# Kernel optimization log

Measured on AMD Instinct MI355X. Metric: run time of the kernel, lower is better.

The kernel has to match this reference:

```python
import jax, jax.numpy as jnp
import numpy as np

N = 50000; E = 800000; T = 800000; G = 64
H = 128; IEMB = 128; BAS = 8; NS = 4; NR = 6; OEH = 128; OUT = 1; NB = 4; CUT = 5.0


def envelope(x):
    # exponent=5 -> p=6: 1/x + a*x^5 + b*x^6 + c*x^7 with a=-28, b=48, c=-21
    return 1.0 / x - 28.0 * x**5 + 48.0 * x**6 - 21.0 * x**7


def setup_inputs() -> dict:
    key = jax.random.key(0)
    ks = iter(jax.random.split(key, 80))
    def w(shape, s=0.1):
        return jax.random.normal(next(ks), shape, dtype=jnp.float32) * s
    inp = {}
    inp['z'] = jax.random.randint(next(ks), (N,), 0, 100, dtype=jnp.int32)
    inp['dist'] = jax.random.uniform(next(ks), (E,), jnp.float32, 0.05, 1.0)
    inp['dist_trip'] = jax.random.uniform(next(ks), (T,), jnp.float32, 0.05, 1.0)
    inp['angle'] = jax.random.uniform(next(ks), (T,), jnp.float32, -1.0, 1.0)
    inp['edge_index'] = jax.random.randint(next(ks), (2, E), 0, N, dtype=jnp.int32)
    inp['triplets'] = jax.random.randint(next(ks), (T, 3), 0, N, dtype=jnp.int32)
    inp['batch'] = jnp.sort(jax.random.randint(next(ks), (N,), 0, G, dtype=jnp.int32))
    inp['atom_table'] = w((100, H), 1.0)
    inp['rbf_freq'] = jnp.arange(1, NR + 1, dtype=jnp.float32) * jnp.float32(np.pi)
    inp['sbf_freq'] = jnp.arange(1, NR + 1, dtype=jnp.float32) * jnp.float32(np.pi)
    inp['emb_w1'] = w((NR, IEMB)); inp['emb_b1'] = w((IEMB,), 0.01)
    inp['emb_w2'] = w((IEMB, H)); inp['emb_b2'] = w((H,), 0.01)
    inp['iw_rbf1'] = w((NB, NR, BAS)); inp['iw_rbf2'] = w((NB, BAS, H))
    inp['iw_sbf1'] = w((NB, NS * NR, BAS)); inp['iw_sbf2'] = w((NB, BAS, IEMB))
    inp['iw_t1'] = w((NB, H, IEMB)); inp['iw_t2'] = w((NB, IEMB, H)); inp['ib_t2'] = w((NB, H), 0.01)
    inp['iw_up'] = w((NB, H, H)); inp['ib_up'] = w((NB, H), 0.01)
    inp['iw_down'] = w((NB, H, H)); inp['ib_down'] = w((NB, H), 0.01)
    inp['ow_rbf'] = w((NB + 1, NR, H))
    inp['ow0'] = w((NB + 1, H, OEH)); inp['ob0'] = w((NB + 1, OEH), 0.01)
    inp['ow1'] = w((NB + 1, OEH, OEH)); inp['ob1'] = w((NB + 1, OEH), 0.01)
    inp['ow2'] = w((NB + 1, OEH, OUT)); inp['ob2'] = w((NB + 1, OUT), 0.01)
    return inp


def _forward(atom_table, rbf_freq, sbf_freq, emb_w1, emb_b1, emb_w2, emb_b2,
             iw_rbf1, iw_rbf2, iw_sbf1, iw_sbf2, iw_t1, iw_t2, ib_t2,
             iw_up, ib_up, iw_down, ib_down, ow_rbf, ow0, ob0, ow1, ob1, ow2, ob2,
             dist, dist_trip, angle, z, edge_index, triplets, batch):
    row, col = edge_index[0], edge_index[1]
    j_idx = triplets[:, 1]
    # radial basis for edges: [E, NR]
    d = dist[:, None] / CUT
    rbf_e = envelope(d) * jnp.sin(rbf_freq * d)
    # spherical basis for triplets: [T, NS*NR]
    dt = dist_trip[:, None] / CUT
    rbf_t = envelope(dt) * jnp.sin(sbf_freq * dt)
    a = angle[:, None]
    sph = jnp.concatenate([jnp.ones_like(a), a, 0.5 * (3 * a**2 - 1), 0.5 * (5 * a**3 - 3 * a)], axis=-1)
    sbf_t = (rbf_t[:, None, :] * sph[:, :, None]).reshape(a.shape[0], -1)

    x = atom_table[z]  # [N, H]
    # EmbeddingBlock: edge msg from rbf only, scattered to col
    e = jax.nn.silu(rbf_e @ emb_w1 + emb_b1) @ emb_w2 + emb_b2
    x = x + jax.ops.segment_sum(e, col, num_segments=N)

    def out_block(k, x):
        rbf_emb = rbf_e @ ow_rbf[k]            # [E, H]
        h = jax.ops.segment_sum(x[row] * rbf_emb, col, num_segments=N)
        h = jax.nn.silu(h @ ow0[k] + ob0[k])
        h = jax.nn.silu(h @ ow1[k] + ob1[k])
        return h @ ow2[k] + ob2[k]             # [N, OUT]

    P = out_block(0, x)
    for b in range(NB):
        x_up = x @ iw_up[b] + ib_up[b]
        x_down = x @ iw_down[b] + ib_down[b]
        rbf_emb = jax.nn.silu(rbf_e @ iw_rbf1[b]) @ iw_rbf2[b]      # [E, H]
        x_edge = x_up[row] * rbf_emb                                  # [E, H]
        sbf_emb = jax.nn.silu(sbf_t @ iw_sbf1[b]) @ iw_sbf2[b]      # [T, H]
        t = jax.nn.silu(x_down @ iw_t1[b]) @ iw_t2[b] + ib_t2[b]     # [N, H]
        # original: for each triplet i, x_edge += t[j]*sbf_emb[i] (broadcast over all edges)
        extra = jnp.sum(t[j_idx] * sbf_emb, axis=0)                   # [H]
        x_edge = x_edge + extra
        x = x + jax.ops.segment_sum(x_edge, col, num_segments=N)
        P = P + out_block(b + 1, x)

    counts = jax.ops.segment_sum(jnp.ones((x.shape[0],), jnp.float32), batch, num_segments=G)
    pooled = jax.ops.segment_sum(P, batch, num_segments=G) / jnp.maximum(counts, 1.0)[:, None]
    return pooled  # [G, OUT]


def reference(z, dist, dist_trip, angle, edge_index, triplets, batch, atom_table, rbf_freq, sbf_freq,
              emb_w1, emb_b1, emb_w2, emb_b2, iw_rbf1, iw_rbf2, iw_sbf1, iw_sbf2, iw_t1, iw_t2, ib_t2,
              iw_up, ib_up, iw_down, ib_down, ow_rbf, ow0, ob0, ow1, ob1, ow2, ob2):
    return _forward(atom_table, rbf_freq, sbf_freq, emb_w1, emb_b1, emb_w2, emb_b2,
                    iw_rbf1, iw_rbf2, iw_sbf1, iw_sbf2, iw_t1, iw_t2, ib_t2,
                    iw_up, ib_up, iw_down, ib_down, ow_rbf, ow0, ob0, ow1, ob1, ow2, ob2,
                    dist, dist_trip, angle, z, edge_index, triplets, batch)
```

## Files before the change

### kernel.cpp

```cpp
#include <hip/hip_runtime.h>
#include <hip/hip_fp16.h>

#define N_ 50000
#define E_ 800000
#define T_ 800000
#define G_ 64
#define H_ 128

#define NBK 782
#define NSB (NBK * 8)
#define CAPS 512
#define CHUNK 4096
#define EB ((E_ + CHUNK - 1) / CHUNK)
#define TB ((T_ + CHUNK - 1) / CHUNK)
#define XSLOT 16

typedef __attribute__((ext_vector_type(8))) short bf16x8;
typedef __attribute__((ext_vector_type(4))) float f32x4;
typedef _Float16 f16x2 __attribute__((ext_vector_type(2)));

__device__ __forceinline__ float siluf(float v) {
    return __fdividef(v, 1.0f + __expf(-v));
}

__device__ __forceinline__ unsigned short f2bf(float f) {
    unsigned int u = __float_as_uint(f);
    u += 0x7fffu + ((u >> 16) & 1u);
    return (unsigned short)(u >> 16);
}
__device__ __forceinline__ unsigned int f2bf2(float a, float b) {
    return (unsigned int)f2bf(a) | ((unsigned int)f2bf(b) << 16);
}
__device__ __forceinline__ float bf2f(unsigned short h) {
    return __uint_as_float(((unsigned int)h) << 16);
}
__device__ __forceinline__ float2 bf2x2(unsigned int p) {
    return make_float2(__uint_as_float(p << 16), __uint_as_float(p & 0xffff0000u));
}
__device__ __forceinline__ float fdot2f(f16x2 a, f16x2 b, float c) {
    return __builtin_amdgcn_fdot2(a, b, c, false);
}

__global__ __launch_bounds__(256) void k_bucket(const int* __restrict__ ecol,
                                                const int* __restrict__ trip,
                                                int* bcntE, unsigned int* __restrict__ ebkt,
                                                int* bcntT, unsigned int* __restrict__ tbkt) {
    __shared__ int hist[NBK];
    __shared__ int bbase[NBK];
    int blk = blockIdx.x;
    bool isE = blk < EB;
    int ebase = (isE ? blk : blk - EB) * CHUNK;
    const int nElem = isE ? E_ : T_;
    int r = blk & 7;
    int* bcnt = isE ? bcntE : bcntT;
    unsigned int* bkt = isE ? ebkt : tbkt;
    int tid = threadIdx.x;

    for (int i = tid; i < NBK; i += 256) hist[i] = 0;
    __syncthreads();

    int cols[16];
    #pragma unroll
    for (int u = 0; u < 16; ++u) {
        int idx = ebase + u * 256 + tid;
        int c = -1;
        if (idx < nElem) c = isE ? ecol[idx] : trip[3 * idx + 1];
        cols[u] = c;
        if (c >= 0) atomicAdd(&hist[c >> 6], 1);
    }
    __syncthreads();

    for (int b = tid; b < NBK; b += 256) {
        int c = hist[b];
        bbase[b] = c ? atomicAdd(&bcnt[b * 8 + r], c) : 0;
        hist[b] = 0;
    }
    __syncthreads();

    #pragma unroll
    for (int u = 0; u < 16; ++u) {
        int c = cols[u];
        if (c >= 0) {
            int bk = c >> 6;
            int off = atomicAdd(&hist[bk], 1);
            int pos = bbase[bk] + off;
            if (pos < CAPS) {
                int idx = ebase + u * 256 + tid;
                bkt[(size_t)(bk * 8 + r) * CAPS + pos] =
                    ((unsigned int)idx << 6) | (unsigned int)(c & 63);
            }
        }
    }
}

__global__ __launch_bounds__(1024) void k_scanB(const int* __restrict__ bcntE, int* bktbaseE,
                                                const int* __restrict__ bcntT, int* bktbaseT) {
    const int* bcnt = (blockIdx.x == 0) ? bcntE : bcntT;
    int* bb = (blockIdx.x == 0) ? bktbaseE : bktbaseT;
    int tid = threadIdx.x, lane = tid & 63, w = tid >> 6;
    __shared__ int wsum[16];
    int v = 0;
    if (tid < NBK) {
        #pragma unroll
        for (int s = 0; s < 8; ++s) v += min(bcnt[tid * 8 + s], CAPS);
    }
    int incl = v;
    #pragma unroll
    for (int s = 1; s < 64; s <<= 1) {
        int t = __shfl_up(incl, (unsigned)s, 64);
        if (lane >= s) incl += t;
    }
    if (lane == 63) wsum[w] = incl;
    __syncthreads();
    int wexcl = 0;
    for (int j = 0; j < w; ++j) wexcl += wsum[j];
    if (tid < NBK) bb[tid] = wexcl + incl - v;
}

__global__ __launch_bounds__(256) void k_place(const int* __restrict__ bcntE, const unsigned int* __restrict__ ebkt,
                                               const int* __restrict__ erow, const float* __restrict__ dist,
                                               const int* __restrict__ bktbaseE, int* __restrict__ rowptrE,
                                               int* __restrict__ slist, float* __restrict__ distS,
                                               const int* __restrict__ bcntT, const unsigned int* __restrict__ tbkt,
                                               const float* __restrict__ dist_trip, const float* __restrict__ angle,
                                               const int* __restrict__ bktbaseT, int* __restrict__ rowptrT,
                                               float2* __restrict__ tpay) {
    int b = blockIdx.x;
    bool isE = b < NBK;
    if (!isE) b -= NBK;
    int tid = threadIdx.x;
    __shared__ int ccnt[64];
    __shared__ int cbase[64];
    __shared__ int nb[8];
    if (tid < 64) ccnt[tid] = 0;
    const int* bcnt = isE ? bcntE : bcntT;
    const unsigned int* bkt = isE ? ebkt : tbkt;
    if (tid < 8) nb[tid] = min(bcnt[b * 8 + tid], CAPS);
    __syncthreads();
    for (int s = 0; s < 8; ++s) {
        int n = nb[s];
        const unsigned int* src = bkt + (size_t)(b * 8 + s) * CAPS;
        for (int i = tid; i < n; i += 256) atomicAdd(&ccnt[src[i] & 63u], 1);
    }
    __syncthreads();
    if (tid < 64) {
        int v = ccnt[tid];
        int incl = v;
        #pragma unroll
        for (int s = 1; s < 64; s <<= 1) {
            int t = __shfl_up(incl, (unsigned)s, 64);
            if (tid >= s) incl += t;
        }
        int base = (isE ? bktbaseE : bktbaseT)[b];
        int excl = base + incl - v;
        cbase[tid] = excl;
        int col = b * 64 + tid;
        int* rp = isE ? rowptrE : rowptrT;
        if (col <= N_) rp[col] = excl;
        ccnt[tid] = 0;
    }
    __syncthreads();
    for (int s = 0; s < 8; ++s) {
        int n = nb[s];
        const unsigned int* src = bkt + (size_t)(b * 8 + s) * CAPS;
        for (int i = tid; i < n; i += 256) {
            unsigned int rec = src[i];
            int c = (int)(rec & 63u);
            int e = (int)(rec >> 6);
            int off = atomicAdd(&ccnt[c], 1);
            int pos = cbase[c] + off;
            if (isE) {
                slist[pos] = erow[e];
                distS[pos] = dist[e];
            } else {
                tpay[pos] = make_float2(dist_trip[e], angle[e]);
            }
        }
    }
}

__global__ __launch_bounds__(256) void k_wprep(const float* __restrict__ emb_w2, const float* __restrict__ iw_down,
                                               const float* __restrict__ iw_t1, const float* __restrict__ iw_t2,
                                               const float* __restrict__ iw_up, const float* __restrict__ ow0,
                                               const float* __restrict__ ow1, unsigned short* __restrict__ Wt) {
    int mat = blockIdx.x >> 3;
    int part = blockIdx.x & 7;
    const float* src;
    if (mat == 0) src = emb_w2;
    else if (mat < 5) src = iw_down + (size_t)(mat - 1) * 16384;
    else if (mat < 9) src = iw_t1 + (size_t)(mat - 5) * 16384;
    else if (mat < 13) src = iw_t2 + (size_t)(mat - 9) * 16384;
    else if (mat < 17) src = iw_up + (size_t)(mat - 13) * 16384;
    else if (mat < 22) src = ow0 + (size_t)(mat - 17) * 16384;
    else src = ow1 + (size_t)(mat - 22) * 16384;
    unsigned short* dst = Wt + (size_t)mat * 16384;
    int base = part * 2048;
    for (int i = base + threadIdx.x; i < base + 2048; i += 256) {
        int k = i >> 7, n = i & 127;
        dst[n * 128 + k] = f2bf(src[i]);
    }
}

__global__ __launch_bounds__(256) void k_geom(const float* __restrict__ distS,
                                              const float* __restrict__ freq, const float* __restrict__ iw_rbf1,
                                              float* __restrict__ rbfS, __half* __restrict__ s8all, int n) {
    __shared__ float W1s[4][48];
    int tid = threadIdx.x;
    if (tid < 192) W1s[tid / 48][tid % 48] = iw_rbf1[tid];
    __syncthreads();
    int p = blockIdx.x * 256 + tid;
    if (p >= n) return;
    float d = distS[p] * 0.2f;
    float d2 = d * d, d4 = d2 * d2, d5 = d4 * d;
    float env = __fdividef(1.0f, d) - 28.0f * d5 + 48.0f * d5 * d - 21.0f * d5 * d2;
    float rb[6];
    #pragma unroll
    for (int r = 0; r < 6; ++r) {
        rb[r] = env * __sinf(freq[r] * d);
        rbfS[(size_t)p * 6 + r] = rb[r];
    }
    #pragma unroll
    for (int b = 0; b < 4; ++b) {
        __half out[8];
        #pragma unroll
        for (int k = 0; k < 8; ++k) {
            float u = 0.f;
            #pragma unroll
            for (int r = 0; r < 6; ++r) u += rb[r] * W1s[b][r * 8 + k];
            out[k] = __float2half(siluf(u));
        }
        *(uint4*)&s8all[((size_t)b * n + p) * 8] = *(uint4*)out;
    }
}

__global__ __launch_bounds__(256) void k_basis(const float2* __restrict__ tpay,
                                               const float* __restrict__ sfreq, __half* __restrict__ basis, int n) {
    int t = blockIdx.x * 256 + threadIdx.x;
    if (t >= n) return;
    float2 da = tpay[t];
    float d = da.x * 0.2f;
    float a = da.y;
    float d2 = d * d, d4 = d2 * d2, d5 = d4 * d;
    float env = __fdividef(1.0f, d) - 28.0f * d5 + 48.0f * d5 * d - 21.0f * d5 * d2;
    float rb[6];
    #pragma unroll
    for (int r = 0; r < 6; ++r) rb[r] = env * __sinf(sfreq[r] * d);
    float sph[4];
    sph[0] = 1.0f; sph[1] = a; sph[2] = 1.5f * a * a - 0.5f; sph[3] = 2.5f * a * a * a - 1.5f * a;
    __half out[24];
    #pragma unroll
    for (int s = 0; s < 4; ++s)
        #pragma unroll
        for (int r = 0; r < 6; ++r) out[s * 6 + r] = __float2half(sph[s] * rb[r]);
    uint4* dst = (uint4*)(basis + (size_t)t * 24);
    dst[0] = ((uint4*)out)[0];
    dst[1] = ((uint4*)out)[1];
    dst[2] = ((uint4*)out)[2];
}

__global__ __launch_bounds__(256) void k_sv4(const int* __restrict__ rowptrT, const __half* __restrict__ basis,
                                             const float* __restrict__ iw_sbf1, float* __restrict__ SV4, int n) {
    int wave = threadIdx.x >> 6, lane = threadIdx.x & 63;
    int node = blockIdx.x * 8 + wave * 2 + (lane >> 5);
    int sub = lane & 31;
    int blk = sub >> 3, k = sub & 7;
    if (node >= n) return;
    const float* W1 = iw_sbf1 + blk * 192;
    f16x2 w[12];
    #pragma unroll
    for (int j = 0; j < 12; ++j) {
        f16x2 t;
        t.x = (_Float16)W1[(2 * j) * 8 + k];
        t.y = (_Float16)W1[(2 * j + 1) * 8 + k];
        w[j] = t;
    }
    float acc = 0.f;
    int p0 = rowptrT[node], p1 = rowptrT[node + 1];
    for (int p = p0; p < p1; ++p) {
        union { uint4 q[3]; f16x2 h[12]; } bs;
        const uint4* bp = (const uint4*)(basis + (size_t)p * 24);
        bs.q[0] = bp[0]; bs.q[1] = bp[1]; bs.q[2] = bp[2];
        float u = 0.f;
        #pragma unroll
        for (int j = 0; j < 12; ++j) u = fdot2f(bs.h[j], w[j], u);
        acc += siluf(u);
    }
    SV4[((size_t)blk * n + node) * 8 + k] = acc;
}

__global__ __launch_bounds__(256) void k_init_x(const float* __restrict__ atab, const int* __restrict__ z,
                                                unsigned short* __restrict__ xh, int n) {
    int t = blockIdx.x * 256 + threadIdx.x;
    if (t >= n * 16) return;
    int node = t >> 4, q = t & 15;
    const float4* a4 = (const float4*)atab;
    float4 v0 = a4[(size_t)z[node] * 32 + q * 2];
    float4 v1 = a4[(size_t)z[node] * 32 + q * 2 + 1];
    uint4 pk;
    pk.x = f2bf2(v0.x, v0.y);
    pk.y = f2bf2(v0.z, v0.w);
    pk.z = f2bf2(v1.x, v1.y);
    pk.w = f2bf2(v1.z, v1.w);
    ((uint4*)xh)[t] = pk;
}

__global__ __launch_bounds__(256) void k_embS(const int* __restrict__ rowptr, const float* __restrict__ rbfS,
                                              const float* __restrict__ w1, const float* __restrict__ b1,
                                              unsigned short* __restrict__ SSh, int n) {
    int node = blockIdx.x * 4 + (threadIdx.x >> 6);
    int lane = threadIdx.x & 63;
    if (node >= n) return;
    int c = lane * 2;
    float wc0[6], wc1[6];
    #pragma unroll
    for (int r = 0; r < 6; ++r) { wc0[r] = w1[r * 128 + c]; wc1[r] = w1[r * 128 + c + 1]; }
    float bb0 = b1[c], bb1 = b1[c + 1];
    float a0 = 0.f, a1 = 0.f;
    int p0 = rowptr[node], p1 = rowptr[node + 1];
    for (int p = p0; p < p1; ++p) {
        const float2* r2 = (const float2*)&rbfS[(size_t)p * 6];
        float2 ra = r2[0], rbx = r2[1], rc = r2[2];
        float u0 = bb0 + ra.x * wc0[0] + ra.y * wc0[1] + rbx.x * wc0[2] + rbx.y * wc0[3] + rc.x * wc0[4] + rc.y * wc0[5];
        float u1 = bb1 + ra.x * wc1[0] + ra.y * wc1[1] + rbx.x * wc1[2] + rbx.y * wc1[3] + rc.x * wc1[4] + rc.y * wc1[5];
        a0 += siluf(u0);
        a1 += siluf(u1);
    }
    *(unsigned int*)&SSh[(size_t)node * 128 + c] = f2bf2(a0, a1);
}

template <int BIAS_MODE, bool SILU, bool ACCBF, bool ABF, bool WF32, bool WBF>
__global__ __launch_bounds__(128) void k_gemm_mfma(const void* __restrict__ Ap,
                                                   const unsigned short* __restrict__ Wt,
                                                   const float* __restrict__ bias, const int* __restrict__ rp,
                                                   float* __restrict__ C, unsigned short* __restrict__ Ch, int M) {
    int tid = threadIdx.x;
    int wave = tid >> 6, lane = tid & 63;
    int m15 = lane & 15, quad = lane >> 4;
    int row0 = blockIdx.x * 32 + wave * 16;
    int arow = row0 + m15;
    if (arow > M - 1) arow = M - 1;

    f32x4 acc[8];
    #pragma unroll
    for (int nt = 0; nt < 8; ++nt) acc[nt] = (f32x4){0.f, 0.f, 0.f, 0.f};

    #pragma unroll
    for (int kt = 0; kt < 4; ++kt) {
        int ks = kt * 32 + quad * 8;
        bf16x8 av;
        if constexpr (ABF) {
            av = *(const bf16x8*)((const unsigned short*)Ap + (size_t)arow * 128 + ks);
        } else {
            const float* Arow = (const float*)Ap + (size_t)arow * 128;
            float4 a0 = *(const float4*)(Arow + ks);
            float4 a1 = *(const float4*)(Arow + ks + 4);
            union { bf16x8 v; unsigned int u[4]; } af;
            af.u[0] = f2bf2(a0.x, a0.y);
            af.u[1] = f2bf2(a0.z, a0.w);
            af.u[2] = f2bf2(a1.x, a1.y);
            af.u[3] = f2bf2(a1.z, a1.w);
            av = af.v;
        }
        #pragma unroll
        for (int nt = 0; nt < 8; ++nt) {
            bf16x8 bf = *(const bf16x8*)(Wt + (size_t)(nt * 16 + m15) * 128 + ks);
            acc[nt] = __builtin_amdgcn_mfma_f32_16x16x32_bf16(av, bf, acc[nt], 0, 0, 0);
        }
    }

    #pragma unroll
    for (int nt = 0; nt < 8; ++nt) {
        int col = nt * 16 + m15;
        float bc = 0.f;
        if constexpr (BIAS_MODE != 0) bc = bias[col];
        #pragma unroll
        for (int reg = 0; reg < 4; ++reg) {
            int row = row0 + quad * 4 + reg;
            if (row < M) {
                float v = acc[nt][reg];
                if constexpr (BIAS_MODE == 1) v += bc;
                if constexpr (BIAS_MODE == 2) v += bc * (float)(rp[row + 1] - rp[row]);
                if constexpr (SILU) v = siluf(v);
                if constexpr (ACCBF) v += bf2f(Ch[(size_t)row * 128 + col]);
                if constexpr (WF32) C[(size_t)row * 128 + col] = v;
                if constexpr (WBF) Ch[(size_t)row * 128 + col] = f2bf(v);
            }
        }
    }
}

template <int PACC>
__global__ __launch_bounds__(128) void k_out_mlp(const unsigned short* __restrict__ hB,
                                                 const unsigned short* __restrict__ W0t, const float* __restrict__ b0,
                                                 const unsigned short* __restrict__ W1t, const float* __restrict__ b1,
                                                 const float* __restrict__ w2col, const float* __restrict__ ob2p,
                                                 float* __restrict__ Pout, int M) {
    __shared__ unsigned short lds[2][16 * 136];
    int tid = threadIdx.x;
    int wave = tid >> 6, lane = tid & 63;
    int m15 = lane & 15, quad = lane >> 4;
    int row0 = blockIdx.x * 32 + wave * 16;
    int arow = row0 + m15;
    if (arow > M - 1) arow = M - 1;
    unsigned short* L = lds[wave];

    f32x4 acc[8];
    #pragma unroll
    for (int nt = 0; nt < 8; ++nt) acc[nt] = (f32x4){0.f, 0.f, 0.f, 0.f};
    #pragma unroll
    for (int kt = 0; kt < 4; ++kt) {
        int ks = kt * 32 + quad * 8;
        bf16x8 av = *(const bf16x8*)(hB + (size_t)arow * 128 + ks);
        #pragma unroll
        for (int nt = 0; nt < 8; ++nt) {
            bf16x8 bf = *(const bf16x8*)(W0t + (size_t)(nt * 16 + m15) * 128 + ks);
            acc[nt] = __builtin_amdgcn_mfma_f32_16x16x32_bf16(av, bf, acc[nt], 0, 0, 0);
        }
    }
    #pragma unroll
    for (int nt = 0; nt < 8; ++nt) {
        int col = nt * 16 + m15;
        float bc = b0[col];
        #pragma unroll
        for (int reg = 0; reg < 4; ++reg)
            L[(quad * 4 + reg) * 136 + col] = f2bf(siluf(acc[nt][reg] + bc));
    }
    __syncthreads();

    #pragma unroll
    for (int nt = 0; nt < 8; ++nt) acc[nt] = (f32x4){0.f, 0.f, 0.f, 0.f};
    #pragma unroll
    for (int kt = 0; kt < 4; ++kt) {
        int ks = kt * 32 + quad * 8;
        bf16x8 av = *(const bf16x8*)(L + m15 * 136 + ks);
        #pragma unroll
        for (int nt = 0; nt < 8; ++nt) {
            bf16x8 bf = *(const bf16x8*)(W1t + (size_t)(nt * 16 + m15) * 128 + ks);
            acc[nt] = __builtin_amdgcn_mfma_f32_16x16x32_bf16(av, bf, acc[nt], 0, 0, 0);
        }
    }
    float w2c[8], pp[4];
    #pragma unroll
    for (int nt = 0; nt < 8; ++nt) w2c[nt] = w2col[nt * 16 + m15];
    #pragma unroll
    for (int reg = 0; reg < 4; ++reg) pp[reg] = 0.f;
    #pragma unroll
    for (int nt = 0; nt < 8; ++nt) {
        float bc = b1[nt * 16 + m15];
        #pragma unroll
        for (int reg = 0; reg < 4; ++reg)
            pp[reg] += siluf(acc[nt][reg] + bc) * w2c[nt];
    }
    #pragma unroll
    for (int reg = 0; reg < 4; ++reg) {
        float s = pp[reg];
        s += __shfl_xor(s, 1, 64);
        s += __shfl_xor(s, 2, 64);
        s += __shfl_xor(s, 4, 64);
        s += __shfl_xor(s, 8, 64);
        if (m15 == 0) {
            int row = row0 + quad * 4 + reg;
            if (row < M) {
                float r = s + ob2p[0];
                if constexpr (PACC == 2) r += Pout[row];
                Pout[row] = r;
            }
        }
    }
}

__global__ __launch_bounds__(128) void k_block_mlp(const unsigned short* __restrict__ xh,
                                                   const unsigned short* __restrict__ Wd, const float* __restrict__ bd,
                                                   const unsigned short* __restrict__ Wt1,
                                                   const unsigned short* __restrict__ Wt2, const float* __restrict__ bt2,
                                                   const unsigned short* __restrict__ Wup, const float* __restrict__ bup,
                                                   const float* __restrict__ SV, const float* __restrict__ W2,
                                                   float* __restrict__ extraP,
                                                   unsigned short* __restrict__ xuph, int M) {
    __shared__ union {
        unsigned short h[2][16 * 136];
        float f[32 * 132];
    } sm;
    int tid = threadIdx.x;
    int wave = tid >> 6, lane = tid & 63;
    int m15 = lane & 15, quad = lane >> 4;
    int row0 = blockIdx.x * 32 + wave * 16;
    int arow = row0 + m15;
    if (arow > M - 1) arow = M - 1;
    unsigned short* L = sm.h[wave];

    f32x4 accD[8], accU[8];
    #pragma unroll
    for (int nt = 0; nt < 8; ++nt) { accD[nt] = (f32x4){0.f, 0.f, 0.f, 0.f}; accU[nt] = (f32x4){0.f, 0.f, 0.f, 0.f}; }
    #pragma unroll
    for (int kt = 0; kt < 4; ++kt) {
        int ks = kt * 32 + quad * 8;
        bf16x8 av = *(const bf16x8*)(xh + (size_t)arow * 128 + ks);
        #pragma unroll
        for (int nt = 0; nt < 8; ++nt) {
            bf16x8 bd_ = *(const bf16x8*)(Wd + (size_t)(nt * 16 + m15) * 128 + ks);
            accD[nt] = __builtin_amdgcn_mfma_f32_16x16x32_bf16(av, bd_, accD[nt], 0, 0, 0);
            bf16x8 bu_ = *(const bf16x8*)(Wup + (size_t)(nt * 16 + m15) * 128 + ks);
            accU[nt] = __builtin_amdgcn_mfma_f32_16x16x32_bf16(av, bu_, accU[nt], 0, 0, 0);
        }
    }
    #pragma unroll
    for (int nt = 0; nt < 8; ++nt) {
        int col = nt * 16 + m15;
        float bcu = bup[col], bcd = bd[col];
        #pragma unroll
        for (int reg = 0; reg < 4; ++reg) {
            int row = row0 + quad * 4 + reg;
            if (row < M) xuph[(size_t)row * 128 + col] = f2bf(accU[nt][reg] + bcu);
            L[(quad * 4 + reg) * 136 + col] = f2bf(accD[nt][reg] + bcd);
        }
    }
    __syncthreads();

    #pragma unroll
    for (int nt = 0; nt < 8; ++nt) accD[nt] = (f32x4){0.f, 0.f, 0.f, 0.f};
    #pragma unroll
    for (int kt = 0; kt < 4; ++kt) {
        int ks = kt * 32 + quad * 8;
        bf16x8 av = *(const bf16x8*)(L + m15 * 136 + ks);
        #pragma unroll
        for (int nt = 0; nt < 8; ++nt) {
            bf16x8 bf = *(const bf16x8*)(Wt1 + (size_t)(nt * 16 + m15) * 128 + ks);
            accD[nt] = __builtin_amdgcn_mfma_f32_16x16x32_bf16(av, bf, accD[nt], 0, 0, 0);
        }
    }
    __syncthreads();
    #pragma unroll
    for (int nt = 0; nt < 8; ++nt) {
        int col = nt * 16 + m15;
        #pragma unroll
        for (int reg = 0; reg < 4; ++reg)
            L[(quad * 4 + reg) * 136 + col] = f2bf(siluf(accD[nt][reg]));
    }
    __syncthreads();

    #pragma unroll
    for (int nt = 0; nt < 8; ++nt) accD[nt] = (f32x4){0.f, 0.f, 0.f, 0.f};
    #pragma unroll
    for (int kt = 0; kt < 4; ++kt) {
        int ks = kt * 32 + quad * 8;
        bf16x8 av = *(const bf16x8*)(L + m15 * 136 + ks);
        #pragma unroll
        for (int nt = 0; nt < 8; ++nt) {
            bf16x8 bf = *(const bf16x8*)(Wt2 + (size_t)(nt * 16 + m15) * 128 + ks);
            accD[nt] = __builtin_amdgcn_mfma_f32_16x16x32_bf16(av, bf, accD[nt], 0, 0, 0);
        }
    }
    __syncthreads();
    #pragma unroll
    for (int nt = 0; nt < 8; ++nt) {
        int col = nt * 16 + m15;
        float bc = bt2[col];
        #pragma unroll
        for (int reg = 0; reg < 4; ++reg) {
            int lr = wave * 16 + quad * 4 + reg;
            sm.f[lr * 132 + col] = accD[nt][reg] + bc;
        }
    }
    __syncthreads();

    int col = tid;
    float acc8[8];
    #pragma unroll
    for (int k = 0; k < 8; ++k) acc8[k] = 0.f;
    int rmax = M - blockIdx.x * 32;
    if (rmax > 32) rmax = 32;
    for (int rr = 0; rr < rmax; ++rr) {
        float t = sm.f[rr * 132 + col];
        const float4* sv4 = (const float4*)&SV[(size_t)(blockIdx.x * 32 + rr) * 8];
        float4 s0 = sv4[0], s1 = sv4[1];
        acc8[0] += t * s0.x; acc8[1] += t * s0.y; acc8[2] += t * s0.z; acc8[3] += t * s0.w;
        acc8[4] += t * s1.x; acc8[5] += t * s1.y; acc8[6] += t * s1.z; acc8[7] += t * s1.w;
    }
    float e = 0.f;
    #pragma unroll
    for (int k = 0; k < 8; ++k) e += acc8[k] * W2[k * 128 + col];
    atomicAdd(&extraP[(blockIdx.x & (XSLOT - 1)) * 128 + col], e);
}

__global__ __launch_bounds__(256) void k_out_gather(const int* __restrict__ rowptr, const int* __restrict__ slist,
                                                    const float* __restrict__ rbfS,
                                                    const unsigned short* __restrict__ xh,
                                                    const float* __restrict__ wrbf,
                                                    unsigned short* __restrict__ hB, int n) {
    int node = blockIdx.x * 4 + (threadIdx.x >> 6);
    int lane = threadIdx.x & 63;
    if (node >= n) return;
    int c = lane * 2;
    float wc0[6], wc1[6];
    #pragma unroll
    for (int r = 0; r < 6; ++r) { wc0[r] = wrbf[r * 128 + c]; wc1[r] = wrbf[r * 128 + c + 1]; }
    float a0 = 0.f, a1 = 0.f;
    int p0 = rowptr[node], p1 = rowptr[node + 1];
    int p = p0;
    for (; p + 4 <= p1; p += 4) {
        int s0 = slist[p], s1 = slist[p + 1], s2 = slist[p + 2], s3 = slist[p + 3];
        float2 rb[4][3];
        #pragma unroll
        for (int u = 0; u < 4; ++u) {
            const float2* r2 = (const float2*)&rbfS[(size_t)(p + u) * 6];
            rb[u][0] = r2[0]; rb[u][1] = r2[1]; rb[u][2] = r2[2];
        }
        unsigned int xv0 = *(const unsigned int*)&xh[(size_t)s0 * 128 + c];
        unsigned int xv1 = *(const unsigned int*)&xh[(size_t)s1 * 128 + c];
        unsigned int xv2 = *(const unsigned int*)&xh[(size_t)s2 * 128 + c];
        unsigned int xv3 = *(const unsigned int*)&xh[(size_t)s3 * 128 + c];
        #pragma unroll
        for (int u = 0; u < 4; ++u) {
            float e0 = rb[u][0].x * wc0[0] + rb[u][0].y * wc0[1] + rb[u][1].x * wc0[2] +
                       rb[u][1].y * wc0[3] + rb[u][2].x * wc0[4] + rb[u][2].y * wc0[5];
            float e1 = rb[u][0].x * wc1[0] + rb[u][0].y * wc1[1] + rb[u][1].x * wc1[2] +
                       rb[u][1].y * wc1[3] + rb[u][2].x * wc1[4] + rb[u][2].y * wc1[5];
            float2 xf = bf2x2((u == 0) ? xv0 : (u == 1) ? xv1 : (u == 2) ? xv2 : xv3);
            a0 += xf.x * e0;
            a1 += xf.y * e1;
        }
    }
    for (; p < p1; ++p) {
        int src = slist[p];
        const float2* r2 = (const float2*)&rbfS[(size_t)p * 6];
        float2 ra = r2[0], rbx = r2[1], rc = r2[2];
        float e0 = ra.x * wc0[0] + ra.y * wc0[1] + rbx.x * wc0[2] + rbx.y * wc0[3] + rc.x * wc0[4] + rc.y * wc0[5];
        float e1 = ra.x * wc1[0] + ra.y * wc1[1] + rbx.x * wc1[2] + rbx.y * wc1[3] + rc.x * wc1[4] + rc.y * wc1[5];
        float2 xf = bf2x2(*(const unsigned int*)&xh[(size_t)src * 128 + c]);
        a0 += xf.x * e0;
        a1 += xf.y * e1;
    }
    *(unsigned int*)&hB[(size_t)node * 128 + c] = f2bf2(a0, a1);
}

__global__ __launch_bounds__(256) void k_interact(const int* __restrict__ rowptr, const int* __restrict__ slist,
                                                  const __half* __restrict__ s8, const float* __restrict__ W2,
                                                  const float* __restrict__ extraP,
                                                  const unsigned short* __restrict__ xuph,
                                                  unsigned short* __restrict__ xh, int n) {
    __shared__ float exs[128];
    int tid = threadIdx.x;
    if (tid < 128) {
        float s = 0.f;
        #pragma unroll
        for (int q = 0; q < XSLOT; ++q) s += extraP[q * 128 + tid];
        exs[tid] = s;
    }
    __syncthreads();
    int node = blockIdx.x * 4 + (tid >> 6);
    int lane = tid & 63;
    if (node >= n) return;
    int c = lane * 2;
    f16x2 w2a[4], w2b[4];
    #pragma unroll
    for (int j = 0; j < 4; ++j) {
        f16x2 wa, wb;
        wa.x = (_Float16)W2[(2 * j) * 128 + c];
        wa.y = (_Float16)W2[(2 * j + 1) * 128 + c];
        wb.x = (_Float16)W2[(2 * j) * 128 + c + 1];
        wb.y = (_Float16)W2[(2 * j + 1) * 128 + c + 1];
        w2a[j] = wa;
        w2b[j] = wb;
    }
    int p0 = rowptr[node], p1 = rowptr[node + 1];
    float cntf = (float)(p1 - p0);
    float a0 = cntf * exs[c], a1 = cntf * exs[c + 1];
    int p = p0;
    for (; p + 4 <= p1; p += 4) {
        int s0 = slist[p], s1 = slist[p + 1], s2 = slist[p + 2], s3 = slist[p + 3];
        uint4 sv[4];
        #pragma unroll
        for (int u = 0; u < 4; ++u) sv[u] = *(const uint4*)(s8 + (size_t)(p + u) * 8);
        unsigned int xv0 = *(const unsigned int*)&xuph[(size_t)s0 * 128 + c];
        unsigned int xv1 = *(const unsigned int*)&xuph[(size_t)s1 * 128 + c];
        unsigned int xv2 = *(const unsigned int*)&xuph[(size_t)s2 * 128 + c];
        unsigned int xv3 = *(const unsigned int*)&xuph[(size_t)s3 * 128 + c];
        #pragma unroll
        for (int u = 0; u < 4; ++u) {
            union { uint4 q; f16x2 h[4]; } s;
            s.q = sv[u];
            float e0 = fdot2f(s.h[0], w2a[0], 0.f);
            e0 = fdot2f(s.h[1], w2a[1], e0);
            e0 = fdot2f(s.h[2], w2a[2], e0);
            e0 = fdot2f(s.h[3], w2a[3], e0);
            float e1 = fdot2f(s.h[0], w2b[0], 0.f);
            e1 = fdot2f(s.h[1], w2b[1], e1);
            e1 = fdot2f(s.h[2], w2b[2], e1);
            e1 = fdot2f(s.h[3], w2b[3], e1);
            float2 xf = bf2x2((u == 0) ? xv0 : (u == 1) ? xv1 : (u == 2) ? xv2 : xv3);
            a0 += xf.x * e0;
            a1 += xf.y * e1;
        }
    }
    for (; p < p1; ++p) {
        int src = slist[p];
        float2 xf = bf2x2(*(const unsigned int*)&xuph[(size_t)src * 128 + c]);
        union { uint4 q; f16x2 h[4]; } s;
        s.q = *(const uint4*)(s8 + (size_t)p * 8);
        float e0 = fdot2f(s.h[0], w2a[0], 0.f);
        e0 = fdot2f(s.h[1], w2a[1], e0);
        e0 = fdot2f(s.h[2], w2a[2], e0);
        e0 = fdot2f(s.h[3], w2a[3], e0);
        float e1 = fdot2f(s.h[0], w2b[0], 0.f);
        e1 = fdot2f(s.h[1], w2b[1], e1);
        e1 = fdot2f(s.h[2], w2b[2], e1);
        e1 = fdot2f(s.h[3], w2b[3], e1);
        a0 += xf.x * e0;
        a1 += xf.y * e1;
    }
    unsigned int cur = *(unsigned int*)&xh[(size_t)node * 128 + c];
    float2 xc = bf2x2(cur);
    *(unsigned int*)&xh[(size_t)node * 128 + c] = f2bf2(xc.x + a0, xc.y + a1);
}

__global__ __launch_bounds__(256) void k_pool(const float* __restrict__ P, const int* __restrict__ batch,
                                              float* __restrict__ pool, float* __restrict__ cnt, int n) {
    int i = blockIdx.x * 256 + threadIdx.x;
    int lane = threadIdx.x & 63;
    int b = (i < n) ? batch[i] : -1;
    float p = (i < n) ? P[i] : 0.f;
    int b0 = __shfl(b, 0, 64);
    int b63 = __shfl(b, 63, 64);
    if (b0 == b63 && b0 >= 0) {
        float s = p;
        #pragma unroll
        for (int off = 32; off > 0; off >>= 1) s += __shfl_xor(s, off, 64);
        if (lane == 0) {
            atomicAdd(&pool[b0], s);
            atomicAdd(&cnt[b0], 64.0f);
        }
    } else {
        if (i < n) {
            atomicAdd(&pool[b], p);
            atomicAdd(&cnt[b], 1.0f);
        }
    }
}

__global__ __launch_bounds__(64) void k_final(const float* __restrict__ pool, const float* __restrict__ cnt,
                                              float* __restrict__ out) {
    int g = threadIdx.x;
    if (g < G_) out[g] = __fdividef(pool[g], fmaxf(cnt[g], 1.0f));
}

extern "C" void kernel_launch(void* const* d_in, const int* in_sizes, int n_in,
                              void* d_out, int out_size, void* d_ws, size_t ws_size,
                              hipStream_t stream) {
    (void)in_sizes; (void)n_in; (void)out_size; (void)ws_size;
    const int* z = (const int*)d_in[0];
    const float* dist = (const float*)d_in[1];
    const float* dist_trip = (const float*)d_in[2];
    const float* angle = (const float*)d_in[3];
    const int* edge_index = (const int*)d_in[4];
    const int* triplets = (const int*)d_in[5];
    const int* batch = (const int*)d_in[6];
    const float* atom_table = (const float*)d_in[7];
    const float* rbf_freq = (const float*)d_in[8];
    const float* sbf_freq = (const float*)d_in[9];
    const float* emb_w1 = (const float*)d_in[10];
    const float* emb_b1 = (const float*)d_in[11];
    const float* emb_w2 = (const float*)d_in[12];
    const float* emb_b2 = (const float*)d_in[13];
    const float* iw_rbf1 = (const float*)d_in[14];
    const float* iw_rbf2 = (const float*)d_in[15];
    const float* iw_sbf1 = (const float*)d_in[16];
    const float* iw_sbf2 = (const float*)d_in[17];
    const float* iw_t1 = (const float*)d_in[18];
    const float* iw_t2 = (const float*)d_in[19];
    const float* ib_t2 = (const float*)d_in[20];
    const float* iw_up = (const float*)d_in[21];
    const float* ib_up = (const float*)d_in[22];
    const float* iw_down = (const float*)d_in[23];
    const float* ib_down = (const float*)d_in[24];
    const float* ow_rbf = (const float*)d_in[25];
    const float* ow0 = (const float*)d_in[26];
    const float* ob0 = (const float*)d_in[27];
    const float* ow1 = (const float*)d_in[28];
    const float* ob1 = (const float*)d_in[29];
    const float* ow2 = (const float*)d_in[30];
    const float* ob2 = (const float*)d_in[31];

    const int* erow = edge_index;
    const int* ecol = edge_index + E_;

    float* ws = (float*)d_ws;
    float* bufA = ws;
    float* bufB = bufA + (size_t)N_ * H_;
    float* P = bufB + (size_t)N_ * H_;
    float* rbfS = P + N_;
    float* SV4 = rbfS + (size_t)E_ * 6;
    float* extra4 = SV4 + (size_t)4 * N_ * 8;
    float* pool = extra4 + 4 * XSLOT * 128;
    float* cnt = pool + G_;
    int* bcntE = (int*)(cnt + G_);
    int* bcntT = bcntE + NSB;
    int* bktbaseE = bcntT + NSB;
    int* bktbaseT = bktbaseE + NBK;
    int* rowptr = bktbaseT + NBK;
    int* rowptrT = rowptr + N_ + 1;
    int* slist = rowptrT + N_ + 1;
    float* distS = (float*)(slist + E_);
    uintptr_t tp = (uintptr_t)(distS + E_);
    tp = (tp + 7) & ~(uintptr_t)7;
    float2* tpay = (float2*)tp;
    __half* s8all = (__half*)(tpay + T_);
    __half* basis = s8all + (size_t)4 * E_ * 8;
    unsigned short* xh = (unsigned short*)(basis + (size_t)T_ * 24);
    unsigned short* xuph = xh + (size_t)N_ * H_;
    unsigned short* Wt = xuph + (size_t)N_ * H_;
    unsigned short* hB = (unsigned short*)bufB;

    unsigned int* ebkt = (unsigned int*)s8all;
    unsigned int* tbkt = ebkt + (size_t)NSB * CAPS;

    const int EG = (E_ + 255) / 256;
    const int TG = (T_ + 255) / 256;
    const int NG4 = (N_ + 3) / 4;
    const int GEMMG2 = (N_ + 31) / 32;

    hipMemsetAsync(extra4, 0, (4 * XSLOT * 128 + 2 * G_ + 2 * NSB) * sizeof(float), stream);
    k_wprep<<<27 * 8, 256, 0, stream>>>(emb_w2, iw_down, iw_t1, iw_t2, iw_up, ow0, ow1, Wt);
    k_bucket<<<EB + TB, 256, 0, stream>>>(ecol, triplets, bcntE, ebkt, bcntT, tbkt);
    k_scanB<<<2, 1024, 0, stream>>>(bcntE, bktbaseE, bcntT, bktbaseT);
    k_place<<<2 * NBK, 256, 0, stream>>>(bcntE, ebkt, erow, dist, bktbaseE, rowptr, slist, distS,
                                         bcntT, tbkt, dist_trip, angle, bktbaseT, rowptrT, tpay);

    k_geom<<<EG, 256, 0, stream>>>(distS, rbf_freq, iw_rbf1, rbfS, s8all, E_);
    k_basis<<<TG, 256, 0, stream>>>(tpay, sbf_freq, basis, T_);
    k_sv4<<<(N_ + 7) / 8, 256, 0, stream>>>(rowptrT, basis, iw_sbf1, SV4, N_);
    k_init_x<<<(N_ * 16 + 255) / 256, 256, 0, stream>>>(atom_table, z, xh, N_);

    k_embS<<<NG4, 256, 0, stream>>>(rowptr, rbfS, emb_w1, emb_b1, (unsigned short*)bufA, N_);
    k_gemm_mfma<2, false, true, true, false, true><<<GEMMG2, 128, 0, stream>>>(
        bufA, Wt, emb_b2, rowptr, nullptr, xh, N_);

    auto out_block = [&](int k, bool first) {
        k_out_gather<<<NG4, 256, 0, stream>>>(rowptr, slist, rbfS, xh,
                                              ow_rbf + (size_t)k * 6 * 128, hB, N_);
        if (first)
            k_out_mlp<1><<<GEMMG2, 128, 0, stream>>>(hB, Wt + (size_t)(17 + k) * 16384, ob0 + k * 128,
                                                     Wt + (size_t)(22 + k) * 16384, ob1 + k * 128,
                                                     ow2 + k * 128, ob2 + k, P, N_);
        else
            k_out_mlp<2><<<GEMMG2, 128, 0, stream>>>(hB, Wt + (size_t)(17 + k) * 16384, ob0 + k * 128,
                                                     Wt + (size_t)(22 + k) * 16384, ob1 + k * 128,
                                                     ow2 + k * 128, ob2 + k, P, N_);
    };

    out_block(0, true);

    for (int b = 0; b < 4; ++b) {
        k_block_mlp<<<GEMMG2, 128, 0, stream>>>(xh,
                                                Wt + (size_t)(1 + b) * 16384, ib_down + b * 128,
                                                Wt + (size_t)(5 + b) * 16384,
                                                Wt + (size_t)(9 + b) * 16384, ib_t2 + b * 128,
                                                Wt + (size_t)(13 + b) * 16384, ib_up + b * 128,
                                                SV4 + (size_t)b * N_ * 8,
                                                iw_sbf2 + (size_t)b * 1024,
                                                extra4 + (size_t)b * XSLOT * 128,
                                                xuph, N_);
        k_interact<<<NG4, 256, 0, stream>>>(rowptr, slist, s8all + (size_t)b * E_ * 8,
                                            iw_rbf2 + (size_t)b * 1024, extra4 + (size_t)b * XSLOT * 128,
                                            xuph, xh, N_);
        out_block(b + 1, false);
    }

    k_pool<<<(N_ + 255) / 256, 256, 0, stream>>>(P, batch, pool, cnt, N_);
    k_final<<<1, 64, 0, stream>>>(pool, cnt, (float*)d_out);
}
```

Before: 1.441 ms.

## Merge independent kernels into combined launches to overlap work across the pipeline

```diff
diff --git a/kernel.cpp b/kernel.cpp
--- a/kernel.cpp
+++ b/kernel.cpp
@@ -14,6 +14,13 @@
 #define EB ((E_ + CHUNK - 1) / CHUNK)
 #define TB ((T_ + CHUNK - 1) / CHUNK)
 #define XSLOT 16
+
+#define GEMMG2 ((N_ + 31) / 32)
+#define NG2 ((N_ + 1) / 2)
+#define NIX ((N_ * 16 + 127) / 128)
+#define SVG ((N_ + 3) / 4)
+#define EG ((E_ + 255) / 256)
+#define TG ((T_ + 255) / 256)
 
 typedef __attribute__((ext_vector_type(8))) short bf16x8;
 typedef __attribute__((ext_vector_type(4))) float f32x4;
@@ -201,67 +208,168 @@
     }
 }
 
-__global__ __launch_bounds__(256) void k_geom(const float* __restrict__ distS,
-                                              const float* __restrict__ freq, const float* __restrict__ iw_rbf1,
-                                              float* __restrict__ rbfS, __half* __restrict__ s8all, int n) {
+__global__ __launch_bounds__(256) void k_geomb(const float* __restrict__ distS,
+                                               const float* __restrict__ freq, const float* __restrict__ iw_rbf1,
+                                               float* __restrict__ rbfS, __half* __restrict__ s8all,
+                                               const float2* __restrict__ tpay, const float* __restrict__ sfreq,
+                                               __half* __restrict__ basis) {
     __shared__ float W1s[4][48];
     int tid = threadIdx.x;
-    if (tid < 192) W1s[tid / 48][tid % 48] = iw_rbf1[tid];
-    __syncthreads();
-    int p = blockIdx.x * 256 + tid;
-    if (p >= n) return;
-    float d = distS[p] * 0.2f;
-    float d2 = d * d, d4 = d2 * d2, d5 = d4 * d;
-    float env = __fdividef(1.0f, d) - 28.0f * d5 + 48.0f * d5 * d - 21.0f * d5 * d2;
-    float rb[6];
-    #pragma unroll
-    for (int r = 0; r < 6; ++r) {
-        rb[r] = env * __sinf(freq[r] * d);
-        rbfS[(size_t)p * 6 + r] = rb[r];
-    }
-    #pragma unroll
-    for (int b = 0; b < 4; ++b) {
-        __half out[8];
-        #pragma unroll
-        for (int k = 0; k < 8; ++k) {
-            float u = 0.f;
+    if (blockIdx.x < EG) {
+        if (tid < 192) W1s[tid / 48][tid % 48] = iw_rbf1[tid];
+        __syncthreads();
+        int p = blockIdx.x * 256 + tid;
+        if (p >= E_) return;
+        float d = distS[p] * 0.2f;
+        float d2 = d * d, d4 = d2 * d2, d5 = d4 * d;
+        float env = __fdividef(1.0f, d) - 28.0f * d5 + 48.0f * d5 * d - 21.0f * d5 * d2;
+        float rb[6];
+        #pragma unroll
+        for (int r = 0; r < 6; ++r) {
+            rb[r] = env * __sinf(freq[r] * d);
+            rbfS[(size_t)p * 6 + r] = rb[r];
+        }
+        #pragma unroll
+        for (int b = 0; b < 4; ++b) {
+            __half out[8];
             #pragma unroll
-            for (int r = 0; r < 6; ++r) u += rb[r] * W1s[b][r * 8 + k];
-            out[k] = __float2half(siluf(u));
-        }
-        *(uint4*)&s8all[((size_t)b * n + p) * 8] = *(uint4*)out;
-    }
-}
-
-__global__ __launch_bounds__(256) void k_basis(const float2* __restrict__ tpay,
-                                               const float* __restrict__ sfreq, __half* __restrict__ basis, int n) {
-    int t = blockIdx.x * 256 + threadIdx.x;
-    if (t >= n) return;
-    float2 da = tpay[t];
-    float d = da.x * 0.2f;
-    float a = da.y;
-    float d2 = d * d, d4 = d2 * d2, d5 = d4 * d;
-    float env = __fdividef(1.0f, d) - 28.0f * d5 + 48.0f * d5 * d - 21.0f * d5 * d2;
-    float rb[6];
-    #pragma unroll
-    for (int r = 0; r < 6; ++r) rb[r] = env * __sinf(sfreq[r] * d);
-    float sph[4];
-    sph[0] = 1.0f; sph[1] = a; sph[2] = 1.5f * a * a - 0.5f; sph[3] = 2.5f * a * a * a - 1.5f * a;
-    __half out[24];
-    #pragma unroll
-    for (int s = 0; s < 4; ++s)
-        #pragma unroll
-        for (int r = 0; r < 6; ++r) out[s * 6 + r] = __float2half(sph[s] * rb[r]);
-    uint4* dst = (uint4*)(basis + (size_t)t * 24);
-    dst[0] = ((uint4*)out)[0];
-    dst[1] = ((uint4*)out)[1];
-    dst[2] = ((uint4*)out)[2];
-}
-
-__global__ __launch_bounds__(256) void k_sv4(const int* __restrict__ rowptrT, const __half* __restrict__ basis,
-                                             const float* __restrict__ iw_sbf1, float* __restrict__ SV4, int n) {
-    int wave = threadIdx.x >> 6, lane = threadIdx.x & 63;
-    int node = blockIdx.x * 8 + wave * 2 + (lane >> 5);
+            for (int k = 0; k < 8; ++k) {
+                float u = 0.f;
+                #pragma unroll
+                for (int r = 0; r < 6; ++r) u += rb[r] * W1s[b][r * 8 + k];
+                out[k] = __float2half(siluf(u));
+            }
+            *(uint4*)&s8all[((size_t)b * E_ + p) * 8] = *(uint4*)out;
+        }
+    } else {
+        int t = (blockIdx.x - EG) * 256 + tid;
+        if (t >= T_) return;
+        float2 da = tpay[t];
+        float d = da.x * 0.2f;
+        float a = da.y;
+        float d2 = d * d, d4 = d2 * d2, d5 = d4 * d;
+        float env = __fdividef(1.0f, d) - 28.0f * d5 + 48.0f * d5 * d - 21.0f * d5 * d2;
+        float rb[6];
+        #pragma unroll
+        for (int r = 0; r < 6; ++r) rb[r] = env * __sinf(sfreq[r] * d);
+        float sph[4];
+        sph[0] = 1.0f; sph[1] = a; sph[2] = 1.5f * a * a - 0.5f; sph[3] = 2.5f * a * a * a - 1.5f * a;
+        __half out[24];
+        #pragma unroll
+        for (int s = 0; s < 4; ++s)
+            #pragma unroll
+            for (int r = 0; r < 6; ++r) out[s * 6 + r] = __float2half(sph[s] * rb[r]);
+        uint4* dst = (uint4*)(basis + (size_t)t * 24);
+        dst[0] = ((uint4*)out)[0];
+        dst[1] = ((uint4*)out)[1];
+        dst[2] = ((uint4*)out)[2];
+    }
+}
+
+__global__ __launch_bounds__(128) void k_embSix(const float* __restrict__ atab, const int* __restrict__ z,
+                                                unsigned short* __restrict__ xh,
+                                                const int* __restrict__ rowptr, const float* __restrict__ rbfS,
+                                                const float* __restrict__ w1, const float* __restrict__ b1,
+                                                unsigned short* __restrict__ SSh) {
+    int tid = threadIdx.x;
+    if (blockIdx.x < NIX) {
+        int t = blockIdx.x * 128 + tid;
+        if (t >= N_ * 16) return;
+        int node = t >> 4, q = t & 15;
+        const float4* a4 = (const float4*)atab;
+        float4 v0 = a4[(size_t)z[node] * 32 + q * 2];
+        float4 v1 = a4[(size_t)z[node] * 32 + q * 2 + 1];
+        uint4 pk;
+        pk.x = f2bf2(v0.x, v0.y);
+        pk.y = f2bf2(v0.z, v0.w);
+        pk.z = f2bf2(v1.x, v1.y);
+        pk.w = f2bf2(v1.z, v1.w);
+        ((uint4*)xh)[t] = pk;
+    } else {
+        int node = (blockIdx.x - NIX) * 2 + (tid >> 6);
+        int lane = tid & 63;
+        if (node >= N_) return;
+        int c = lane * 2;
+        float wc0[6], wc1[6];
+        #pragma unroll
+        for (int r = 0; r < 6; ++r) { wc0[r] = w1[r * 128 + c]; wc1[r] = w1[r * 128 + c + 1]; }
+        float bb0 = b1[c], bb1 = b1[c + 1];
+        float a0 = 0.f, a1 = 0.f;
+        int p0 = rowptr[node], p1 = rowptr[node + 1];
+        int p = p0;
+        for (; p + 4 <= p1; p += 4) {
+            float2 rb[4][3];
+            #pragma unroll
+            for (int u = 0; u < 4; ++u) {
+                const float2* r2 = (const float2*)&rbfS[(size_t)(p + u) * 6];
+                rb[u][0] = r2[0]; rb[u][1] = r2[1]; rb[u][2] = r2[2];
+            }
+            #pragma unroll
+            for (int u = 0; u < 4; ++u) {
+                float u0 = bb0 + rb[u][0].x * wc0[0] + rb[u][0].y * wc0[1] + rb[u][1].x * wc0[2] +
+                           rb[u][1].y * wc0[3] + rb[u][2].x * wc0[4] + rb[u][2].y * wc0[5];
+                float u1 = bb1 + rb[u][0].x * wc1[0] + rb[u][0].y * wc1[1] + rb[u][1].x * wc1[2] +
+                           rb[u][1].y * wc1[3] + rb[u][2].x * wc1[4] + rb[u][2].y * wc1[5];
+                a0 += siluf(u0);
+                a1 += siluf(u1);
+            }
+        }
+        for (; p < p1; ++p) {
+            const float2* r2 = (const float2*)&rbfS[(size_t)p * 6];
+            float2 ra = r2[0], rbx = r2[1], rc = r2[2];
+            float u0 = bb0 + ra.x * wc0[0] + ra.y * wc0[1] + rbx.x * wc0[2] + rbx.y * wc0[3] + rc.x * wc0[4] + rc.y * wc0[5];
+            float u1 = bb1 + ra.x * wc1[0] + ra.y * wc1[1] + rbx.x * wc1[2] + rbx.y * wc1[3] + rc.x * wc1[4] + rc.y * wc1[5];
+            a0 += siluf(u0);
+            a1 += siluf(u1);
+        }
+        *(unsigned int*)&SSh[(size_t)node * 128 + c] = f2bf2(a0, a1);
+    }
+}
+
+
+__device__ __forceinline__ void body_gemm(int bid, const unsigned short* Ap, const unsigned short* Wt,
+                                          const float* bias, const int* rp, unsigned short* Ch, int M) {
+    int tid = threadIdx.x;
+    int wave = tid >> 6, lane = tid & 63;
+    int m15 = lane & 15, quad = lane >> 4;
+    int row0 = bid * 32 + wave * 16;
+    int arow = row0 + m15;
+    if (arow > M - 1) arow = M - 1;
+
+    f32x4 acc[8];
+    #pragma unroll
+    for (int nt = 0; nt < 8; ++nt) acc[nt] = (f32x4){0.f, 0.f, 0.f, 0.f};
+    #pragma unroll
+    for (int kt = 0; kt < 4; ++kt) {
+        int ks = kt * 32 + quad * 8;
+        bf16x8 av = *(const bf16x8*)(Ap + (size_t)arow * 128 + ks);
+        #pragma unroll
+        for (int nt = 0; nt < 8; ++nt) {
+            bf16x8 bf = *(const bf16x8*)(Wt + (size_t)(nt * 16 + m15) * 128 + ks);
+            acc[nt] = __builtin_amdgcn_mfma_f32_16x16x32_bf16(av, bf, acc[nt], 0, 0, 0);
+        }
+    }
+    #pragma unroll
+    for (int nt = 0; nt < 8; ++nt) {
+        int col = nt * 16 + m15;
+        float bc = bias[col];
+        #pragma unroll
+        for (int reg = 0; reg < 4; ++reg) {
+            int row = row0 + quad * 4 + reg;
+            if (row < M) {
+                float v = acc[nt][reg] + bc * (float)(rp[row + 1] - rp[row]);
+                v += bf2f(Ch[(size_t)row * 128 + col]);
+                Ch[(size_t)row * 128 + col] = f2bf(v);
+            }
+        }
+    }
+}
+
+__device__ __forceinline__ void body_sv4(int bid, const int* rowptrT, const __half* basis,
+                                         const float* iw_sbf1, float* SV4, int n) {
+    int tid = threadIdx.x;
+    int wave = tid >> 6, lane = tid & 63;
+    int node = bid * 4 + wave * 2 + (lane >> 5);
     int sub = lane & 31;
     int blk = sub >> 3, k = sub & 7;
     if (node >= n) return;
@@ -288,121 +396,178 @@
     SV4[((size_t)blk * n + node) * 8 + k] = acc;
 }
 
-__global__ __launch_bounds__(256) void k_init_x(const float* __restrict__ atab, const int* __restrict__ z,
-                                                unsigned short* __restrict__ xh, int n) {
-    int t = blockIdx.x * 256 + threadIdx.x;
-    if (t >= n * 16) return;
-    int node = t >> 4, q = t & 15;
-    const float4* a4 = (const float4*)atab;
-    float4 v0 = a4[(size_t)z[node] * 32 + q * 2];
-    float4 v1 = a4[(size_t)z[node] * 32 + q * 2 + 1];
-    uint4 pk;
-    pk.x = f2bf2(v0.x, v0.y);
-    pk.y = f2bf2(v0.z, v0.w);
-    pk.z = f2bf2(v1.x, v1.y);
-    pk.w = f2bf2(v1.z, v1.w);
-    ((uint4*)xh)[t] = pk;
-}
-
-__global__ __launch_bounds__(256) void k_embS(const int* __restrict__ rowptr, const float* __restrict__ rbfS,
-                                              const float* __restrict__ w1, const float* __restrict__ b1,
-                                              unsigned short* __restrict__ SSh, int n) {
-    int node = blockIdx.x * 4 + (threadIdx.x >> 6);
-    int lane = threadIdx.x & 63;
+__device__ __forceinline__ void body_gather(int node0, const int* rowptr, const int* slist,
+                                            const float* rbfS, const unsigned short* xh,
+                                            const float* wrbf, unsigned short* hB, int n) {
+    int tid = threadIdx.x;
+    int node = node0 + (tid >> 6);
+    int lane = tid & 63;
     if (node >= n) return;
     int c = lane * 2;
     float wc0[6], wc1[6];
     #pragma unroll
-    for (int r = 0; r < 6; ++r) { wc0[r] = w1[r * 128 + c]; wc1[r] = w1[r * 128 + c + 1]; }
-    float bb0 = b1[c], bb1 = b1[c + 1];
+    for (int r = 0; r < 6; ++r) { wc0[r] = wrbf[r * 128 + c]; wc1[r] = wrbf[r * 128 + c + 1]; }
     float a0 = 0.f, a1 = 0.f;
     int p0 = rowptr[node], p1 = rowptr[node + 1];
-    for (int p = p0; p < p1; ++p) {
+    int p = p0;
+    for (; p + 4 <= p1; p += 4) {
+        int s0 = slist[p], s1 = slist[p + 1], s2 = slist[p + 2], s3 = slist[p + 3];
+        float2 rb[4][3];
+        #pragma unroll
+        for (int u = 0; u < 4; ++u) {
+            const float2* r2 = (const float2*)&rbfS[(size_t)(p + u) * 6];
+            rb[u][0] = r2[0]; rb[u][1] = r2[1]; rb[u][2] = r2[2];
+        }
+        unsigned int xv0 = *(const unsigned int*)&xh[(size_t)s0 * 128 + c];
+        unsigned int xv1 = *(const unsigned int*)&xh[(size_t)s1 * 128 + c];
+        unsigned int xv2 = *(const unsigned int*)&xh[(size_t)s2 * 128 + c];
+        unsigned int xv3 = *(const unsigned int*)&xh[(size_t)s3 * 128 + c];
+        #pragma unroll
+        for (int u = 0; u < 4; ++u) {
+            float e0 = rb[u][0].x * wc0[0] + rb[u][0].y * wc0[1] + rb[u][1].x * wc0[2] +
+                       rb[u][1].y * wc0[3] + rb[u][2].x * wc0[4] + rb[u][2].y * wc0[5];
+            float e1 = rb[u][0].x * wc1[0] + rb[u][0].y * wc1[1] + rb[u][1].x * wc1[2] +
+                       rb[u][1].y * wc1[3] + rb[u][2].x * wc1[4] + rb[u][2].y * wc1[5];
+            float2 xf = bf2x2((u == 0) ? xv0 : (u == 1) ? xv1 : (u == 2) ? xv2 : xv3);
+            a0 += xf.x * e0;
+            a1 += xf.y * e1;
+        }
+    }
+    for (; p < p1; ++p) {
+        int src = slist[p];
         const float2* r2 = (const float2*)&rbfS[(size_t)p * 6];
         float2 ra = r2[0], rbx = r2[1], rc = r2[2];
-        float u0 = bb0 + ra.x * wc0[0] + ra.y * wc0[1] + rbx.x * wc0[2] + rbx.y * wc0[3] + rc.x * wc0[4] + rc.y * wc0[5];
-        float u1 = bb1 + ra.x * wc1[0] + ra.y * wc1[1] + rbx.x * wc1[2] + rbx.y * wc1[3] + rc.x * wc1[4] + rc.y * wc1[5];
-        a0 += siluf(u0);
-        a1 += siluf(u1);
-    }
-    *(unsigned int*)&SSh[(size_t)node * 128 + c] = f2bf2(a0, a1);
-}
-
-template <int BIAS_MODE, bool SILU, bool ACCBF, bool ABF, bool WF32, bool WBF>
-__global__ __launch_bounds__(128) void k_gemm_mfma(const void* __restrict__ Ap,
-                                                   const unsigned short* __restrict__ Wt,
-                                                   const float* __restrict__ bias, const int* __restrict__ rp,
-                                                   float* __restrict__ C, unsigned short* __restrict__ Ch, int M) {
+        float e0 = ra.x * wc0[0] + ra.y * wc0[1] + rbx.x * wc0[2] + rbx.y * wc0[3] + rc.x * wc0[4] + rc.y * wc0[5];
+        float e1 = ra.x * wc1[0] + ra.y * wc1[1] + rbx.x * wc1[2] + rbx.y * wc1[3] + rc.x * wc1[4] + rc.y * wc1[5];
+        float2 xf = bf2x2(*(const unsigned int*)&xh[(size_t)src * 128 + c]);
+        a0 += xf.x * e0;
+        a1 += xf.y * e1;
+    }
+    *(unsigned int*)&hB[(size_t)node * 128 + c] = f2bf2(a0, a1);
+}
+
+__device__ __forceinline__ void body_block_mlp(int bid, unsigned short* smh,
+                                               const unsigned short* xh,
+                                               const unsigned short* Wd, const float* bd,
+                                               const unsigned short* Wt1,
+                                               const unsigned short* Wt2, const float* bt2,
+                                               const unsigned short* Wup, const float* bup,
+                                               const float* SV, const float* W2,
+                                               float* extraP, unsigned short* xuph, int M) {
     int tid = threadIdx.x;
     int wave = tid >> 6, lane = tid & 63;
     int m15 = lane & 15, quad = lane >> 4;
-    int row0 = blockIdx.x * 32 + wave * 16;
+    int row0 = bid * 32 + wave * 16;
     int arow = row0 + m15;
     if (arow > M - 1) arow = M - 1;
-
-    f32x4 acc[8];
-    #pragma unroll
-    for (int nt = 0; nt < 8; ++nt) acc[nt] = (f32x4){0.f, 0.f, 0.f, 0.f};
-
+    unsigned short* L = smh + wave * (16 * 136);
+
+    f32x4 accD[8], accU[8];
+    #pragma unroll
+    for (int nt = 0; nt < 8; ++nt) { accD[nt] = (f32x4){0.f, 0.f, 0.f, 0.f}; accU[nt] = (f32x4){0.f, 0.f, 0.f, 0.f}; }
     #pragma unroll
     for (int kt = 0; kt < 4; ++kt) {
         int ks = kt * 32 + quad * 8;
-        bf16x8 av;
-        if constexpr (ABF) {
-            av = *(const bf16x8*)((const unsigned short*)Ap + (size_t)arow * 128 + ks);
-        } else {
-            const float* Arow = (const float*)Ap + (size_t)arow * 128;
-            float4 a0 = *(const float4*)(Arow + ks);
-            float4 a1 = *(const float4*)(Arow + ks + 4);
-            union { bf16x8 v; unsigned int u[4]; } af;
-            af.u[0] = f2bf2(a0.x, a0.y);
-            af.u[1] = f2bf2(a0.z, a0.w);
-            af.u[2] = f2bf2(a1.x, a1.y);
-            af.u[3] = f2bf2(a1.z, a1.w);
-            av = af.v;
-        }
+        bf16x8 av = *(const bf16x8*)(xh + (size_t)arow * 128 + ks);
         #pragma unroll
         for (int nt = 0; nt < 8; ++nt) {
-            bf16x8 bf = *(const bf16x8*)(Wt + (size_t)(nt * 16 + m15) * 128 + ks);
-            acc[nt] = __builtin_amdgcn_mfma_f32_16x16x32_bf16(av, bf, acc[nt], 0, 0, 0);
-        }
-    }
-
+            bf16x8 bd_ = *(const bf16x8*)(Wd + (size_t)(nt * 16 + m15) * 128 + ks);
+            accD[nt] = __builtin_amdgcn_mfma_f32_16x16x32_bf16(av, bd_, accD[nt], 0, 0, 0);
+            bf16x8 bu_ = *(const bf16x8*)(Wup + (size_t)(nt * 16 + m15) * 128 + ks);
+            accU[nt] = __builtin_amdgcn_mfma_f32_16x16x32_bf16(av, bu_, accU[nt], 0, 0, 0);
+        }
+    }
     #pragma unroll
     for (int nt = 0; nt < 8; ++nt) {
         int col = nt * 16 + m15;
-        float bc = 0.f;
-        if constexpr (BIAS_MODE != 0) bc = bias[col];
+        float bcu = bup[col], bcd = bd[col];
         #pragma unroll
         for (int reg = 0; reg < 4; ++reg) {
             int row = row0 + quad * 4 + reg;
-            if (row < M) {
-                float v = acc[nt][reg];
-                if constexpr (BIAS_MODE == 1) v += bc;
-                if constexpr (BIAS_MODE == 2) v += bc * (float)(rp[row + 1] - rp[row]);
-                if constexpr (SILU) v = siluf(v);
-                if constexpr (ACCBF) v += bf2f(Ch[(size_t)row * 128 + col]);
-                if constexpr (WF32) C[(size_t)row * 128 + col] = v;
-                if constexpr (WBF) Ch[(size_t)row * 128 + col] = f2bf(v);
-            }
-        }
-    }
+            if (row < M) xuph[(size_t)row * 128 + col] = f2bf(accU[nt][reg] + bcu);
+            L[(quad * 4 + reg) * 136 + col] = f2bf(accD[nt][reg] + bcd);
+        }
+    }
+    __syncthreads();
+
+    #pragma unroll
+    for (int nt = 0; nt < 8; ++nt) accD[nt] = (f32x4){0.f, 0.f, 0.f, 0.f};
+    #pragma unroll
+    for (int kt = 0; kt < 4; ++kt) {
+        int ks = kt * 32 + quad * 8;
+        bf16x8 av = *(const bf16x8*)(L + m15 * 136 + ks);
+        #pragma unroll
+        for (int nt = 0; nt < 8; ++nt) {
+            bf16x8 bf = *(const bf16x8*)(Wt1 + (size_t)(nt * 16 + m15) * 128 + ks);
+            accD[nt] = __builtin_amdgcn_mfma_f32_16x16x32_bf16(av, bf, accD[nt], 0, 0, 0);
+        }
+    }
+    __syncthreads();
+    #pragma unroll
+    for (int nt = 0; nt < 8; ++nt) {
+        int col = nt * 16 + m15;
+        #pragma unroll
+        for (int reg = 0; reg < 4; ++reg)
+            L[(quad * 4 + reg) * 136 + col] = f2bf(siluf(accD[nt][reg]));
+    }
+    __syncthreads();
+
+    #pragma unroll
+    for (int nt = 0; nt < 8; ++nt) accD[nt] = (f32x4){0.f, 0.f, 0.f, 0.f};
+    #pragma unroll
+    for (int kt = 0; kt < 4; ++kt) {
+        int ks = kt * 32 + quad * 8;
+        bf16x8 av = *(const bf16x8*)(L + m15 * 136 + ks);
+        #pragma unroll
+        for (int nt = 0; nt < 8; ++nt) {
+            bf16x8 bf = *(const bf16x8*)(Wt2 + (size_t)(nt * 16 + m15) * 128 + ks);
+            accD[nt] = __builtin_amdgcn_mfma_f32_16x16x32_bf16(av, bf, accD[nt], 0, 0, 0);
+        }
+    }
+    __syncthreads();
+    #pragma unroll
+    for (int nt = 0; nt < 8; ++nt) {
+        int col = nt * 16 + m15;
+        float bc = bt2[col];
+        #pragma unroll
+        for (int reg = 0; reg < 4; ++reg)
+            smh[(wave * 16 + quad * 4 + reg) * 136 + col] = f2bf(accD[nt][reg] + bc);
+    }
+    __syncthreads();
+
+    int col = tid;
+    float acc8[8];
+    #pragma unroll
+    for (int k = 0; k < 8; ++k) acc8[k] = 0.f;
+    int rmax = M - bid * 32;
+    if (rmax > 32) rmax = 32;
+    for (int rr = 0; rr < rmax; ++rr) {
+        float t = bf2f(smh[rr * 136 + col]);
+        const float4* sv4 = (const float4*)&SV[(size_t)(bid * 32 + rr) * 8];
+        float4 s0 = sv4[0], s1 = sv4[1];
+        acc8[0] += t * s0.x; acc8[1] += t * s0.y; acc8[2] += t * s0.z; acc8[3] += t * s0.w;
+        acc8[4] += t * s1.x; acc8[5] += t * s1.y; acc8[6] += t * s1.z; acc8[7] += t * s1.w;
+    }
+    float e = 0.f;
+    #pragma unroll
+    for (int k = 0; k < 8; ++k) e += acc8[k] * W2[k * 128 + col];
+    atomicAdd(&extraP[(bid & (XSLOT - 1)) * 128 + col], e);
 }
 
 template <int PACC>
-__global__ __launch_bounds__(128) void k_out_mlp(const unsigned short* __restrict__ hB,
-                                                 const unsigned short* __restrict__ W0t, const float* __restrict__ b0,
-                                                 const unsigned short* __restrict__ W1t, const float* __restrict__ b1,
-                                                 const float* __restrict__ w2col, const float* __restrict__ ob2p,
-                                                 float* __restrict__ Pout, int M) {
-    __shared__ unsigned short lds[2][16 * 136];
+__device__ __forceinline__ void body_out_mlp(int bid, unsigned short* smh,
+                                             const unsigned short* hB,
+                                             const unsigned short* W0t, const float* b0,
+                                             const unsigned short* W1t, const float* b1,
+                                             const float* w2col, const float* ob2p,
+                                             float* Pout, int M) {
     int tid = threadIdx.x;
     int wave = tid >> 6, lane = tid & 63;
     int m15 = lane & 15, quad = lane >> 4;
-    int row0 = blockIdx.x * 32 + wave * 16;
+    int row0 = bid * 32 + wave * 16;
     int arow = row0 + m15;
     if (arow > M - 1) arow = M - 1;
-    unsigned short* L = lds[wave];
+    unsigned short* L = smh + wave * (16 * 136);
 
     f32x4 acc[8];
     #pragma unroll
@@ -462,193 +627,28 @@
             int row = row0 + quad * 4 + reg;
             if (row < M) {
                 float r = s + ob2p[0];
-                if constexpr (PACC == 2) r += Pout[row];
+                if (PACC == 2) r += Pout[row];
                 Pout[row] = r;
             }
         }
     }
 }
 
-__global__ __launch_bounds__(128) void k_block_mlp(const unsigned short* __restrict__ xh,
-                                                   const unsigned short* __restrict__ Wd, const float* __restrict__ bd,
-                                                   const unsigned short* __restrict__ Wt1,
-                                                   const unsigned short* __restrict__ Wt2, const float* __restrict__ bt2,
-                                                   const unsigned short* __restrict__ Wup, const float* __restrict__ bup,
-                                                   const float* __restrict__ SV, const float* __restrict__ W2,
-                                                   float* __restrict__ extraP,
-                                                   unsigned short* __restrict__ xuph, int M) {
-    __shared__ union {
-        unsigned short h[2][16 * 136];
-        float f[32 * 132];
-    } sm;
+__device__ __forceinline__ void body_interact(int node0, float* exs,
+                                              const int* rowptr, const int* slist,
+                                              const __half* s8, const float* W2,
+                                              const float* extraP,
+                                              const unsigned short* xuph,
+                                              unsigned short* xh, int n) {
     int tid = threadIdx.x;
-    int wave = tid >> 6, lane = tid & 63;
-    int m15 = lane & 15, quad = lane >> 4;
-    int row0 = blockIdx.x * 32 + wave * 16;
-    int arow = row0 + m15;
-    if (arow > M - 1) arow = M - 1;
-    unsigned short* L = sm.h[wave];
-
-    f32x4 accD[8], accU[8];
-    #pragma unroll
-    for (int nt = 0; nt < 8; ++nt) { accD[nt] = (f32x4){0.f, 0.f, 0.f, 0.f}; accU[nt] = (f32x4){0.f, 0.f, 0.f, 0.f}; }
-    #pragma unroll
-    for (int kt = 0; kt < 4; ++kt) {
-        int ks = kt * 32 + quad * 8;
-        bf16x8 av = *(const bf16x8*)(xh + (size_t)arow * 128 + ks);
-        #pragma unroll
-        for (int nt = 0; nt < 8; ++nt) {
-            bf16x8 bd_ = *(const bf16x8*)(Wd + (size_t)(nt * 16 + m15) * 128 + ks);
-            accD[nt] = __builtin_amdgcn_mfma_f32_16x16x32_bf16(av, bd_, accD[nt], 0, 0, 0);
-            bf16x8 bu_ = *(const bf16x8*)(Wup + (size_t)(nt * 16 + m15) * 128 + ks);
-            accU[nt] = __builtin_amdgcn_mfma_f32_16x16x32_bf16(av, bu_, accU[nt], 0, 0, 0);
-        }
-    }
-    #pragma unroll
-    for (int nt = 0; nt < 8; ++nt) {
-        int col = nt * 16 + m15;
-        float bcu = bup[col], bcd = bd[col];
-        #pragma unroll
-        for (int reg = 0; reg < 4; ++reg) {
-            int row = row0 + quad * 4 + reg;
-            if (row < M) xuph[(size_t)row * 128 + col] = f2bf(accU[nt][reg] + bcu);
-            L[(quad * 4 + reg) * 136 + col] = f2bf(accD[nt][reg] + bcd);
-        }
-    }
-    __syncthreads();
-
-    #pragma unroll
-    for (int nt = 0; nt < 8; ++nt) accD[nt] = (f32x4){0.f, 0.f, 0.f, 0.f};
-    #pragma unroll
-    for (int kt = 0; kt < 4; ++kt) {
-        int ks = kt * 32 + quad * 8;
-        bf16x8 av = *(const bf16x8*)(L + m15 * 136 + ks);
-        #pragma unroll
-        for (int nt = 0; nt < 8; ++nt) {
-            bf16x8 bf = *(const bf16x8*)(Wt1 + (size_t)(nt * 16 + m15) * 128 + ks);
-            accD[nt] = __builtin_amdgcn_mfma_f32_16x16x32_bf16(av, bf, accD[nt], 0, 0, 0);
-        }
-    }
-    __syncthreads();
-    #pragma unroll
-    for (int nt = 0; nt < 8; ++nt) {
-        int col = nt * 16 + m15;
-        #pragma unroll
-        for (int reg = 0; reg < 4; ++reg)
-            L[(quad * 4 + reg) * 136 + col] = f2bf(siluf(accD[nt][reg]));
-    }
-    __syncthreads();
-
-    #pragma unroll
-    for (int nt = 0; nt < 8; ++nt) accD[nt] = (f32x4){0.f, 0.f, 0.f, 0.f};
-    #pragma unroll
-    for (int kt = 0; kt < 4; ++kt) {
-        int ks = kt * 32 + quad * 8;
-        bf16x8 av = *(const bf16x8*)(L + m15 * 136 + ks);
-        #pragma unroll
-        for (int nt = 0; nt < 8; ++nt) {
-            bf16x8 bf = *(const bf16x8*)(Wt2 + (size_t)(nt * 16 + m15) * 128 + ks);
-            accD[nt] = __builtin_amdgcn_mfma_f32_16x16x32_bf16(av, bf, accD[nt], 0, 0, 0);
-        }
-    }
-    __syncthreads();
-    #pragma unroll
-    for (int nt = 0; nt < 8; ++nt) {
-        int col = nt * 16 + m15;
-        float bc = bt2[col];
-        #pragma unroll
-        for (int reg = 0; reg < 4; ++reg) {
-            int lr = wave * 16 + quad * 4 + reg;
-            sm.f[lr * 132 + col] = accD[nt][reg] + bc;
-        }
-    }
-    __syncthreads();
-
-    int col = tid;
-    float acc8[8];
-    #pragma unroll
-    for (int k = 0; k < 8; ++k) acc8[k] = 0.f;
-    int rmax = M - blockIdx.x * 32;
-    if (rmax > 32) rmax = 32;
-    for (int rr = 0; rr < rmax; ++rr) {
-        float t = sm.f[rr * 132 + col];
-        const float4* sv4 = (const float4*)&SV[(size_t)(blockIdx.x * 32 + rr) * 8];
-        float4 s0 = sv4[0], s1 = sv4[1];
-        acc8[0] += t * s0.x; acc8[1] += t * s0.y; acc8[2] += t * s0.z; acc8[3] += t * s0.w;
-        acc8[4] += t * s1.x; acc8[5] += t * s1.y; acc8[6] += t * s1.z; acc8[7] += t * s1.w;
-    }
-    float e = 0.f;
-    #pragma unroll
-    for (int k = 0; k < 8; ++k) e += acc8[k] * W2[k * 128 + col];
-    atomicAdd(&extraP[(blockIdx.x & (XSLOT - 1)) * 128 + col], e);
-}
-
-__global__ __launch_bounds__(256) void k_out_gather(const int* __restrict__ rowptr, const int* __restrict__ slist,
-                                                    const float* __restrict__ rbfS,
-                                                    const unsigned short* __restrict__ xh,
-                                                    const float* __restrict__ wrbf,
-                                                    unsigned short* __restrict__ hB, int n) {
-    int node = blockIdx.x * 4 + (threadIdx.x >> 6);
-    int lane = threadIdx.x & 63;
-    if (node >= n) return;
-    int c = lane * 2;
-    float wc0[6], wc1[6];
-    #pragma unroll
-    for (int r = 0; r < 6; ++r) { wc0[r] = wrbf[r * 128 + c]; wc1[r] = wrbf[r * 128 + c + 1]; }
-    float a0 = 0.f, a1 = 0.f;
-    int p0 = rowptr[node], p1 = rowptr[node + 1];
-    int p = p0;
-    for (; p + 4 <= p1; p += 4) {
-        int s0 = slist[p], s1 = slist[p + 1], s2 = slist[p + 2], s3 = slist[p + 3];
-        float2 rb[4][3];
-        #pragma unroll
-        for (int u = 0; u < 4; ++u) {
-            const float2* r2 = (const float2*)&rbfS[(size_t)(p + u) * 6];
-            rb[u][0] = r2[0]; rb[u][1] = r2[1]; rb[u][2] = r2[2];
-        }
-        unsigned int xv0 = *(const unsigned int*)&xh[(size_t)s0 * 128 + c];
-        unsigned int xv1 = *(const unsigned int*)&xh[(size_t)s1 * 128 + c];
-        unsigned int xv2 = *(const unsigned int*)&xh[(size_t)s2 * 128 + c];
-        unsigned int xv3 = *(const unsigned int*)&xh[(size_t)s3 * 128 + c];
-        #pragma unroll
-        for (int u = 0; u < 4; ++u) {
-            float e0 = rb[u][0].x * wc0[0] + rb[u][0].y * wc0[1] + rb[u][1].x * wc0[2] +
-                       rb[u][1].y * wc0[3] + rb[u][2].x * wc0[4] + rb[u][2].y * wc0[5];
-            float e1 = rb[u][0].x * wc1[0] + rb[u][0].y * wc1[1] + rb[u][1].x * wc1[2] +
-                       rb[u][1].y * wc1[3] + rb[u][2].x * wc1[4] + rb[u][2].y * wc1[5];
-            float2 xf = bf2x2((u == 0) ? xv0 : (u == 1) ? xv1 : (u == 2) ? xv2 : xv3);
-            a0 += xf.x * e0;
-            a1 += xf.y * e1;
-        }
-    }
-    for (; p < p1; ++p) {
-        int src = slist[p];
-        const float2* r2 = (const float2*)&rbfS[(size_t)p * 6];
-        float2 ra = r2[0], rbx = r2[1], rc = r2[2];
-        float e0 = ra.x * wc0[0] + ra.y * wc0[1] + rbx.x * wc0[2] + rbx.y * wc0[3] + rc.x * wc0[4] + rc.y * wc0[5];
-        float e1 = ra.x * wc1[0] + ra.y * wc1[1] + rbx.x * wc1[2] + rbx.y * wc1[3] + rc.x * wc1[4] + rc.y * wc1[5];
-        float2 xf = bf2x2(*(const unsigned int*)&xh[(size_t)src * 128 + c]);
-        a0 += xf.x * e0;
-        a1 += xf.y * e1;
-    }
-    *(unsigned int*)&hB[(size_t)node * 128 + c] = f2bf2(a0, a1);
-}
-
-__global__ __launch_bounds__(256) void k_interact(const int* __restrict__ rowptr, const int* __restrict__ slist,
-                                                  const __half* __restrict__ s8, const float* __restrict__ W2,
-                                                  const float* __restrict__ extraP,
-                                                  const unsigned short* __restrict__ xuph,
-                                                  unsigned short* __restrict__ xh, int n) {
-    __shared__ float exs[128];
-    int tid = threadIdx.x;
-    if (tid < 128) {
+    {
         float s = 0.f;
         #pragma unroll
         for (int q = 0; q < XSLOT; ++q) s += extraP[q * 128 + tid];
         exs[tid] = s;
     }
     __syncthreads();
-    int node = blockIdx.x * 4 + (tid >> 6);
+    int node = node0 + (tid >> 6);
     int lane = tid & 63;
     if (node >= n) return;
     int c = lane * 2;
@@ -712,6 +712,68 @@
     unsigned int cur = *(unsigned int*)&xh[(size_t)node * 128 + c];
     float2 xc = bf2x2(cur);
     *(unsigned int*)&xh[(size_t)node * 128 + c] = f2bf2(xc.x + a0, xc.y + a1);
+}
+
+
+__global__ __launch_bounds__(128) void k_gemmsv(const unsigned short* __restrict__ Ap,
+                                                const unsigned short* __restrict__ Wt,
+                                                const float* __restrict__ bias, const int* __restrict__ rp,
+                                                unsigned short* __restrict__ Ch,
+                                                const int* __restrict__ rowptrT, const __half* __restrict__ basis,
+                                                const float* __restrict__ iw_sbf1, float* __restrict__ SV4) {
+    if (blockIdx.x < GEMMG2)
+        body_gemm(blockIdx.x, Ap, Wt, bias, rp, Ch, N_);
+    else
+        body_sv4(blockIdx.x - GEMMG2, rowptrT, basis, iw_sbf1, SV4, N_);
+}
+
+__global__ __launch_bounds__(128) void k_fuse_gb(const unsigned short* __restrict__ xh,
+                                                 const unsigned short* __restrict__ Wd, const float* __restrict__ bd,
+                                                 const unsigned short* __restrict__ Wt1,
+                                                 const unsigned short* __restrict__ Wt2, const float* __restrict__ bt2,
+                                                 const unsigned short* __restrict__ Wup, const float* __restrict__ bup,
+                                                 const float* __restrict__ SV, const float* __restrict__ W2,
+                                                 float* __restrict__ extraP, unsigned short* __restrict__ xuph,
+                                                 const int* __restrict__ rowptr, const int* __restrict__ slist,
+                                                 const float* __restrict__ rbfS, const float* __restrict__ wrbf,
+                                                 unsigned short* __restrict__ hB) {
+    __shared__ unsigned short smh[2 * 16 * 136];
+    if (blockIdx.x < GEMMG2)
+        body_block_mlp(blockIdx.x, smh, xh, Wd, bd, Wt1, Wt2, bt2, Wup, bup, SV, W2, extraP, xuph, N_);
+    else
+        body_gather((blockIdx.x - GEMMG2) * 2, rowptr, slist, rbfS, xh, wrbf, hB, N_);
+}
+
+template <int PACC>
+__global__ __launch_bounds__(128) void k_fuse_mi(const unsigned short* __restrict__ hB,
+                                                 const unsigned short* __restrict__ W0t, const float* __restrict__ b0,
+                                                 const unsigned short* __restrict__ W1t, const float* __restrict__ b1,
+                                                 const float* __restrict__ w2col, const float* __restrict__ ob2p,
+                                                 float* __restrict__ Pout,
+                                                 const int* __restrict__ rowptr, const int* __restrict__ slist,
+                                                 const __half* __restrict__ s8, const float* __restrict__ W2,
+                                                 const float* __restrict__ extraP,
+                                                 const unsigned short* __restrict__ xuph,
+                                                 unsigned short* __restrict__ xh) {
+    __shared__ unsigned short smh[2 * 16 * 136];
+    if (blockIdx.x < GEMMG2)
+        body_out_mlp<PACC>(blockIdx.x, smh, hB, W0t, b0, W1t, b1, w2col, ob2p, Pout, N_);
+    else
+        body_interact((blockIdx.x - GEMMG2) * 2, (float*)smh, rowptr, slist, s8, W2, extraP, xuph, xh, N_);
+}
+
+__global__ __launch_bounds__(128) void k_gather1(const int* __restrict__ rowptr, const int* __restrict__ slist,
+                                                 const float* __restrict__ rbfS, const unsigned short* __restrict__ xh,
+                                                 const float* __restrict__ wrbf, unsigned short* __restrict__ hB) {
+    body_gather(blockIdx.x * 2, rowptr, slist, rbfS, xh, wrbf, hB, N_);
+}
+__global__ __launch_bounds__(128) void k_mlp1(const unsigned short* __restrict__ hB,
+                                              const unsigned short* __restrict__ W0t, const float* __restrict__ b0,
+                                              const unsigned short* __restrict__ W1t, const float* __restrict__ b1,
+                                              const float* __restrict__ w2col, const float* __restrict__ ob2p,
+                                              float* __restrict__ Pout) {
+    __shared__ unsigned short smh[2 * 16 * 136];
+    body_out_mlp<2>(blockIdx.x, smh, hB, W0t, b0, W1t, b1, w2col, ob2p, Pout, N_);
 }
 
 __global__ __launch_bounds__(256) void k_pool(const float* __restrict__ P, const int* __restrict__ batch,
@@ -814,11 +876,6 @@
     unsigned int* ebkt = (unsigned int*)s8all;
     unsigned int* tbkt = ebkt + (size_t)NSB * CAPS;
 
-    const int EG = (E_ + 255) / 256;
-    const int TG = (T_ + 255) / 256;
-    const int NG4 = (N_ + 3) / 4;
-    const int GEMMG2 = (N_ + 31) / 32;
-
     hipMemsetAsync(extra4, 0, (4 * XSLOT * 128 + 2 * G_ + 2 * NSB) * sizeof(float), stream);
     k_wprep<<<27 * 8, 256, 0, stream>>>(emb_w2, iw_down, iw_t1, iw_t2, iw_up, ow0, ow1, Wt);
     k_bucket<<<EB + TB, 256, 0, stream>>>(ecol, triplets, bcntE, ebkt, bcntT, tbkt);
@@ -826,45 +883,49 @@
     k_place<<<2 * NBK, 256, 0, stream>>>(bcntE, ebkt, erow, dist, bktbaseE, rowptr, slist, distS,
                                          bcntT, tbkt, dist_trip, angle, bktbaseT, rowptrT, tpay);
 
-    k_geom<<<EG, 256, 0, stream>>>(distS, rbf_freq, iw_rbf1, rbfS, s8all, E_);
-    k_basis<<<TG, 256, 0, stream>>>(tpay, sbf_freq, basis, T_);
-    k_sv4<<<(N_ + 7) / 8, 256, 0, stream>>>(rowptrT, basis, iw_sbf1, SV4, N_);
-    k_init_x<<<(N_ * 16 + 255) / 256, 256, 0, stream>>>(atom_table, z, xh, N_);
-
-    k_embS<<<NG4, 256, 0, stream>>>(rowptr, rbfS, emb_w1, emb_b1, (unsigned short*)bufA, N_);
-    k_gemm_mfma<2, false, true, true, false, true><<<GEMMG2, 128, 0, stream>>>(
-        bufA, Wt, emb_b2, rowptr, nullptr, xh, N_);
-
-    auto out_block = [&](int k, bool first) {
-        k_out_gather<<<NG4, 256, 0, stream>>>(rowptr, slist, rbfS, xh,
-                                              ow_rbf + (size_t)k * 6 * 128, hB, N_);
-        if (first)
-            k_out_mlp<1><<<GEMMG2, 128, 0, stream>>>(hB, Wt + (size_t)(17 + k) * 16384, ob0 + k * 128,
-                                                     Wt + (size_t)(22 + k) * 16384, ob1 + k * 128,
-                                                     ow2 + k * 128, ob2 + k, P, N_);
+    k_geomb<<<EG + TG, 256, 0, stream>>>(distS, rbf_freq, iw_rbf1, rbfS, s8all,
+                                         tpay, sbf_freq, basis);
+    k_embSix<<<NIX + NG2, 128, 0, stream>>>(atom_table, z, xh, rowptr, rbfS, emb_w1, emb_b1,
+                                            (unsigned short*)bufA);
+    k_gemmsv<<<GEMMG2 + SVG, 128, 0, stream>>>((unsigned short*)bufA, Wt, emb_b2, rowptr, xh,
+                                               rowptrT, basis, iw_sbf1, SV4);
+
+    for (int b = 0; b < 4; ++b) {
+        k_fuse_gb<<<GEMMG2 + NG2, 128, 0, stream>>>(xh,
+                                                    Wt + (size_t)(1 + b) * 16384, ib_down + b * 128,
+                                                    Wt + (size_t)(5 + b) * 16384,
+                                                    Wt + (size_t)(9 + b) * 16384, ib_t2 + b * 128,
+                                                    Wt + (size_t)(13 + b) * 16384, ib_up + b * 128,
+                                                    SV4 + (size_t)b * N_ * 8,
+                                                    iw_sbf2 + (size_t)b * 1024,
+                                                    extra4 + (size_t)b * XSLOT * 128,
+                                                    xuph,
+                                                    rowptr, slist, rbfS,
+                                                    ow_rbf + (size_t)b * 6 * 128, hB);
+        if (b == 0)
+            k_fuse_mi<1><<<GEMMG2 + NG2, 128, 0, stream>>>(hB,
+                                                           Wt + (size_t)(17 + b) * 16384, ob0 + b * 128,
+                                                           Wt + (size_t)(22 + b) * 16384, ob1 + b * 128,
+                                                           ow2 + b * 128, ob2 + b, P,
+                                                           rowptr, slist, s8all + (size_t)b * E_ * 8,
+                                                           iw_rbf2 + (size_t)b * 1024,
+                                                           extra4 + (size_t)b * XSLOT * 128,
+                                                           xuph, xh);
         else
-            k_out_mlp<2><<<GEMMG2, 128, 0, stream>>>(hB, Wt + (size_t)(17 + k) * 16384, ob0 + k * 128,
-                                                     Wt + (size_t)(22 + k) * 16384, ob1 + k * 128,
-                                                     ow2 + k * 128, ob2 + k, P, N_);
-    };
-
-    out_block(0, true);
-
-    for (int b = 0; b < 4; ++b) {
-        k_block_mlp<<<GEMMG2, 128, 0, stream>>>(xh,
-                                                Wt + (size_t)(1 + b) * 16384, ib_down + b * 128,
-                                                Wt + (size_t)(5 + b) * 16384,
-                                                Wt + (size_t)(9 + b) * 16384, ib_t2 + b * 128,
-                                                Wt + (size_t)(13 + b) * 16384, ib_up + b * 128,
-                                                SV4 + (size_t)b * N_ * 8,
-                                                iw_sbf2 + (size_t)b * 1024,
-                                                extra4 + (size_t)b * XSLOT * 128,
-                                                xuph, N_);
-        k_interact<<<NG4, 256, 0, stream>>>(rowptr, slist, s8all + (size_t)b * E_ * 8,
-                                            iw_rbf2 + (size_t)b * 1024, extra4 + (size_t)b * XSLOT * 128,
-                                            xuph, xh, N_);
-        out_block(b + 1, false);
-    }
+            k_fuse_mi<2><<<GEMMG2 + NG2, 128, 0, stream>>>(hB,
+                                                           Wt + (size_t)(17 + b) * 16384, ob0 + b * 128,
+                                                           Wt + (size_t)(22 + b) * 16384, ob1 + b * 128,
+                                                           ow2 + b * 128, ob2 + b, P,
+                                                           rowptr, slist, s8all + (size_t)b * E_ * 8,
+                                                           iw_rbf2 + (size_t)b * 1024,
+                                                           extra4 + (size_t)b * XSLOT * 128,
+                                                           xuph, xh);
+    }
+
+    k_gather1<<<NG2, 128, 0, stream>>>(rowptr, slist, rbfS, xh, ow_rbf + (size_t)4 * 6 * 128, hB);
+    k_mlp1<<<GEMMG2, 128, 0, stream>>>(hB, Wt + (size_t)21 * 16384, ob0 + 4 * 128,
+                                       Wt + (size_t)26 * 16384, ob1 + 4 * 128,
+                                       ow2 + 4 * 128, ob2 + 4, P);
 
     k_pool<<<(N_ + 255) / 256, 256, 0, stream>>>(P, batch, pool, cnt, N_);
     k_final<<<1, 64, 0, stream>>>(pool, cnt, (float*)d_out);
```

New measurement: 1.533 ms. 1.06x slower.
